# Kernel tuning notes

Measured on AMD Instinct MI355X. Metric: run time of the kernel, lower is better.

## Reference

```python
import math
import jax, jax.numpy as jnp
import numpy as np
from jax.scipy.special import xlogy, gammaln

HEADS = 8
DIM_KEY = 64
NUM_REL_POS_FEATURES = 192


def get_positional_embed(n, feature_size):
    # distances: [-n+1, ..., n-1], length 2n-1
    dist = jnp.arange(-n + 1, n)
    adist = jnp.abs(dist).astype(jnp.float32)[:, None]  # (2n-1, 1)
    num_basis = feature_size // 6  # 3 feature fns * 2 (sign-augmented)
    seq_len = n
    # exponential half-life features
    max_range = math.log(seq_len) / math.log(2.0)
    half_life = 2.0 ** jnp.linspace(3.0, max_range, num_basis)  # min_half_life=3.0
    feat_exp = jnp.exp(-math.log(2.0) / half_life[None, :] * adist)
    # central mask features
    center_widths = 2.0 ** jnp.arange(1, num_basis + 1) - 1.0
    feat_cm = (center_widths[None, :] > adist).astype(jnp.float32)
    # gamma pdf features
    stddev = seq_len / (2 * num_basis)
    start_mean = seq_len / num_basis
    mean = jnp.linspace(start_mean, float(seq_len), num_basis)[None, :]
    concentration = (mean / stddev) ** 2
    rate = mean / (stddev ** 2)
    log_unnorm = xlogy(concentration - 1.0, adist) - rate * adist
    log_norm = gammaln(concentration) - concentration * jnp.log(rate)
    prob = jnp.exp(log_unnorm - log_norm) + 1e-8
    feat_gamma = prob / jnp.max(prob, axis=-1, keepdims=True)
    emb = jnp.concatenate([feat_exp, feat_cm, feat_gamma], axis=-1)  # (2n-1, fs/2)
    sign = jnp.sign(dist).astype(jnp.float32)[:, None]
    return jnp.concatenate([emb, sign * emb], axis=-1)  # (2n-1, fs)


def relative_shift(x):
    # x: (b, h, n, 2n-1) -> (b, h, n, n) Transformer-XL shift
    b, h, t1, t2 = x.shape
    x = jnp.pad(x, ((0, 0), (0, 0), (0, 0), (1, 0)))  # (b,h,t1,t2+1)
    x = x.reshape(b, h, t2 + 1, t1)[:, :, 1:, :].reshape(b, h, t1, t2)
    return x[..., : (t2 + 2) // 2]


def setup_inputs() -> dict:
    key = jax.random.key(0)
    ks = jax.random.split(key, 8)
    dim = 1536
    b, n = 2, 1536
    hdk = HEADS * DIM_KEY  # 512
    hdv = HEADS * 192      # 1536
    s = 0.02
    return {
        'x': jax.random.normal(ks[0], (b, n, dim), jnp.float32),
        'Wq': jax.random.normal(ks[1], (hdk, dim), jnp.float32) * s,
        'Wk': jax.random.normal(ks[2], (hdk, dim), jnp.float32) * s,
        'Wv': jax.random.normal(ks[3], (hdv, dim), jnp.float32) * s,
        'Wrel': jax.random.normal(ks[4], (hdk, NUM_REL_POS_FEATURES), jnp.float32) * s,
        'Wout': jax.random.normal(ks[5], (dim, hdv), jnp.float32) * s,
        'b_out': jnp.zeros((dim,), jnp.float32),
        'rel_content_bias': jax.random.normal(ks[6], (1, HEADS, 1, DIM_KEY), jnp.float32),
        'rel_pos_bias': jax.random.normal(ks[7], (1, HEADS, 1, DIM_KEY), jnp.float32),
    }


def reference(x, Wq, Wk, Wv, Wrel, Wout, b_out, rel_content_bias, rel_pos_bias):
    b, n, dim = x.shape
    h = HEADS
    scale = DIM_KEY ** -0.5

    def split_heads(t):  # (b, n, h*d) -> (b, h, n, d)
        return t.reshape(b, n, h, -1).transpose(0, 2, 1, 3)

    q = split_heads(jnp.einsum('bnd,fd->bnf', x, Wq)) * scale
    k = split_heads(jnp.einsum('bnd,fd->bnf', x, Wk))
    v = split_heads(jnp.einsum('bnd,fd->bnf', x, Wv))

    content_logits = jnp.einsum('bhid,bhjd->bhij', q + rel_content_bias, k)

    positions = get_positional_embed(n, NUM_REL_POS_FEATURES)  # (2n-1, fs)
    rel_k = jnp.einsum('jf,ef->je', positions, Wrel).reshape(2 * n - 1, h, DIM_KEY)
    rel_k = rel_k.transpose(1, 0, 2)  # (h, 2n-1, dk)
    rel_logits = jnp.einsum('bhid,hjd->bhij', q + rel_pos_bias, rel_k)
    rel_logits = relative_shift(rel_logits)  # (b, h, n, n)

    attn = jax.nn.softmax(content_logits + rel_logits, axis=-1)
    out = jnp.einsum('bhij,bhjd->bhid', attn, v)
    out = out.transpose(0, 2, 1, 3).reshape(b, n, -1)  # (b, n, h*dv)
    return jnp.einsum('bnf,df->bnd', out, Wout) + b_out
```

## Files before the change

### kernel.cpp

```cpp
#include <hip/hip_runtime.h>
#include <cmath>

typedef unsigned short u16;
typedef unsigned int u32;
typedef short frag8 __attribute__((ext_vector_type(8)));
typedef float f32x4 __attribute__((ext_vector_type(4)));

#define DEVINL __device__ __forceinline__

DEVINL float bf2f(u16 v) { return __uint_as_float(((u32)v) << 16); }
DEVINL u16 f2bf(float f) {
    u32 u = __float_as_uint(f);
    u32 r = (u + 0x7fffu + ((u >> 16) & 1u)) >> 16;
    return (u16)r;
}
DEVINL u32 pack2(float a, float b) { return (u32)f2bf(a) | ((u32)f2bf(b) << 16); }
DEVINL void async_copy16(const u16* g, u16* l) {
    __builtin_amdgcn_global_load_lds((const __attribute__((address_space(1))) u32*)g,
                                     (__attribute__((address_space(3))) u32*)l, 16, 0, 0);
}
DEVINL f32x4 mfma_bf16(frag8 a, frag8 b, f32x4 c) {
    return __builtin_amdgcn_mfma_f32_16x16x32_bf16(a, b, c, 0, 0, 0);
}

__global__ __launch_bounds__(256) void convert_kernel(
        const float* __restrict__ s0, const float* __restrict__ s1,
        const float* __restrict__ s2, const float* __restrict__ s3,
        const float* __restrict__ s4, u16* __restrict__ dst) {
    const int c0 = 589824, c1 = 98304, c2 = 98304, c3 = 294912;
    const int total = 1376256;
    for (int c = blockIdx.x * blockDim.x + threadIdx.x; c < total;
         c += gridDim.x * blockDim.x) {
        const float* src; int off;
        if (c < c0) { src = s0; off = c; }
        else if (c < c0 + c1) { src = s1; off = c - c0; }
        else if (c < c0 + c1 + c2) { src = s2; off = c - c0 - c1; }
        else if (c < c0 + c1 + c2 + c3) { src = s3; off = c - c0 - c1 - c2; }
        else { src = s4; off = c - c0 - c1 - c2 - c3; }
        float4 a = ((const float4*)src)[off * 2];
        float4 b = ((const float4*)src)[off * 2 + 1];
        uint4 o;
        o.x = pack2(a.x, a.y); o.y = pack2(a.z, a.w);
        o.z = pack2(b.x, b.y); o.w = pack2(b.z, b.w);
        ((uint4*)dst)[c] = o;
    }
}

DEVINL double lgamma_stirling(double z) {
    double zi = 1.0 / z, zi2 = zi * zi;
    return (z - 0.5) * log(z) - z + 0.91893853320467274178
         + zi * (1.0 / 12.0) - zi * zi2 * (1.0 / 360.0) + zi * zi2 * zi2 * (1.0 / 1260.0);
}

__global__ __launch_bounds__(256) void embed_relk_kernel(const float* __restrict__ Wrel,
                                                         u16* __restrict__ relk) {
    __shared__ float pos[16][192];
    __shared__ float inv_hl[32], cwid[32], cm1[32], rateS[32];
    __shared__ double lognS[32];
    __shared__ float gmax[16];
    int t = threadIdx.x;
    int u0b = blockIdx.x * 16;

    if (t < 32) {
        double step = (10.584962500721156 - 3.0) / 31.0;
        double hl = exp2(3.0 + t * step);
        inv_hl[t] = (float)(1.0 / hl);
        cwid[t] = exp2f((float)(t + 1)) - 1.0f;
        double mean = 48.0 * (t + 1);
        double conc = (mean / 24.0) * (mean / 24.0);
        double rate = mean / 576.0;
        cm1[t] = (float)(conc - 1.0);
        rateS[t] = (float)rate;
        lognS[t] = lgamma_stirling(conc) - conc * log(rate);
    }
    __syncthreads();

    for (int idx = t; idx < 512; idx += 256) {
        int ul = idx >> 5, bs = idx & 31;
        int dist = u0b + ul - 1535;
        float ad = fabsf((float)dist);
        pos[ul][bs] = exp2f(-ad * inv_hl[bs]);
        pos[ul][32 + bs] = (cwid[bs] > ad) ? 1.0f : 0.0f;
        double prob = 0.0;
        if (dist != 0) {
            double adD = (double)ad;
            prob = exp((double)cm1[bs] * log(adD) - (double)rateS[bs] * adD - lognS[bs]);
        }
        pos[ul][64 + bs] = (float)(prob + 1e-8);
    }
    __syncthreads();
    if (t < 16) {
        float g = 0.f;
        #pragma unroll
        for (int bsx = 0; bsx < 32; bsx++) g = fmaxf(g, pos[t][64 + bsx]);
        gmax[t] = g;
    }
    __syncthreads();
    for (int idx = t; idx < 16 * 96; idx += 256) {
        int ul = idx / 96, f = idx - ul * 96;
        float v = pos[ul][f];
        if (f >= 64) { v = v / gmax[ul]; pos[ul][f] = v; }
        int dist = u0b + ul - 1535;
        float sg = (dist > 0) ? 1.f : ((dist < 0) ? -1.f : 0.f);
        pos[ul][96 + f] = sg * v;
    }
    __syncthreads();

    int e0 = t * 2;
    const float* w0 = Wrel + e0 * 192;
    const float* w1 = w0 + 192;
    float a0[16], a1[16];
    #pragma unroll
    for (int ul = 0; ul < 16; ul++) { a0[ul] = 0.f; a1[ul] = 0.f; }
    for (int f = 0; f < 192; f++) {
        float wa = w0[f], wb = w1[f];
        #pragma unroll
        for (int ul = 0; ul < 16; ul++) {
            float p = pos[ul][f];
            a0[ul] = fmaf(p, wa, a0[ul]);
            a1[ul] = fmaf(p, wb, a1[ul]);
        }
    }
    int h0 = e0 >> 6, d0 = e0 & 63;
    int h1 = (e0 + 1) >> 6, d1 = (e0 + 1) & 63;
    for (int ul = 0; ul < 16; ul++) {
        int u = u0b + ul;
        relk[(h0 * 3072 + u) * 64 + d0] = f2bf(a0[ul]);
        relk[(h1 * 3072 + u) * 64 + d1] = f2bf(a1[ul]);
    }
}

DEVINL void gemm128_mainloop(const u16* __restrict__ A, const u16* __restrict__ B,
                             int K, f32x4 acc[4][4], u16* As, u16* Bs) {
    int tid = threadIdx.x;
    int lane = tid & 63, wave = tid >> 6;
    int wm = (wave >> 1) * 64, wn = (wave & 1) * 64;
    int fm = lane & 15, fq = lane >> 4;
    for (int k0 = 0; k0 < K; k0 += 32) {
        #pragma unroll
        for (int p = 0; p < 2; p++) {
            int e = (p * 256 + tid) * 8;
            int r = e >> 5, c = e & 31;
            async_copy16(A + r * K + k0 + c, As + e);
            async_copy16(B + r * K + k0 + c, Bs + e);
        }
        __syncthreads();
        frag8 af[4], bfr[4];
        #pragma unroll
        for (int mi = 0; mi < 4; mi++) af[mi] = *(const frag8*)&As[(wm + 16 * mi + fm) * 32 + fq * 8];
        #pragma unroll
        for (int ni = 0; ni < 4; ni++) bfr[ni] = *(const frag8*)&Bs[(wn + 16 * ni + fm) * 32 + fq * 8];
        #pragma unroll
        for (int mi = 0; mi < 4; mi++)
            #pragma unroll
            for (int ni = 0; ni < 4; ni++)
                acc[mi][ni] = mfma_bf16(af[mi], bfr[ni], acc[mi][ni]);
        __syncthreads();
    }
}

__global__ __launch_bounds__(256) void gemm_qkv_kernel(
        const u16* __restrict__ X, const u16* __restrict__ Wq, const u16* __restrict__ Wk,
        const u16* __restrict__ Wv, const float* __restrict__ cbias, const float* __restrict__ pbias,
        u16* __restrict__ qc, u16* __restrict__ qp, u16* __restrict__ kws, u16* __restrict__ vt) {
    __shared__ __align__(16) u16 As[128 * 32];
    __shared__ __align__(16) u16 Bs[128 * 32];
    int m0 = blockIdx.x * 128, n0 = blockIdx.y * 128;
    const u16* Bp; int brow;
    if (n0 < 512)       { Bp = Wq; brow = n0; }
    else if (n0 < 1024) { Bp = Wk; brow = n0 - 512; }
    else                { Bp = Wv; brow = n0 - 1024; }
    f32x4 acc[4][4];
    #pragma unroll
    for (int i = 0; i < 4; i++)
        #pragma unroll
        for (int j = 0; j < 4; j++) acc[i][j] = (f32x4){0.f, 0.f, 0.f, 0.f};
    gemm128_mainloop(X + m0 * 1536, Bp + brow * 1536, 1536, acc, As, Bs);

    int tid = threadIdx.x, lane = tid & 63, wave = tid >> 6;
    int wm = (wave >> 1) * 64, wn = (wave & 1) * 64, fm = lane & 15, fq = lane >> 4;
    #pragma unroll
    for (int mi = 0; mi < 4; mi++) {
        #pragma unroll
        for (int ni = 0; ni < 4; ni++) {
            int col = n0 + wn + 16 * ni + fm;
            int rbase = m0 + wm + 16 * mi + fq * 4;
            #pragma unroll
            for (int reg = 0; reg < 4; reg++) {
                int row = rbase + reg;
                float v = acc[mi][ni][reg];
                int b = row >= 1536 ? 1 : 0;
                int i = row - b * 1536;
                if (n0 < 512) {
                    float qv = v * 0.125f;
                    int idx = ((b * 8 + (col >> 6)) * 1536 + i) * 64 + (col & 63);
                    qc[idx] = f2bf(qv + cbias[col]);
                    qp[idx] = f2bf(qv + pbias[col]);
                } else if (n0 < 1024) {
                    int c2 = col - 512;
                    kws[((b * 8 + (c2 >> 6)) * 1536 + i) * 64 + (c2 & 63)] = f2bf(v);
                } else {
                    int c2 = col - 1024;
                    int hh = c2 / 192, dd = c2 - hh * 192;
                    vt[((b * 8 + hh) * 192 + dd) * 1536 + i] = f2bf(v);
                }
            }
        }
    }
}

__global__ __launch_bounds__(256) void attn_kernel(
        const u16* __restrict__ qc, const u16* __restrict__ qp, const u16* __restrict__ kws,
        const u16* __restrict__ vt, const u16* __restrict__ relk, u16* __restrict__ ao) {
    __shared__ __align__(16) u16 smem[24768];
    u16* k_lds    = smem;
    u16* vt_lds   = smem + 4096;
    u16* relk_lds = smem + 16384;
    u16* P_lds    = smem + 22528;
    float* S_lds  = (float*)k_lds;
    float* R_lds  = (float*)relk_lds;
    float* mstate = (float*)(smem + 24576);
    float* lstate = mstate + 32;
    float* alpha_lds = lstate + 32;

    const int n = 1536;
    int bh = blockIdx.y, b = bh >> 3, h = bh & 7;
    int i0 = blockIdx.x * 32;
    const u16* qcP = qc + bh * n * 64;
    const u16* qpP = qp + bh * n * 64;
    const u16* kP  = kws + bh * n * 64;
    const u16* vtP = vt + bh * 192 * n;
    const u16* rkP = relk + h * 3072 * 64;

    int tid = threadIdx.x, lane = tid & 63, w = tid >> 6, fm = lane & 15, fq = lane >> 4;
    int sw = fm & 7;
    if (tid < 32) { mstate[tid] = __int_as_float(0xff800000); lstate[tid] = 0.f; }

    frag8 aqc[2][2], aqp[2][2];
    #pragma unroll
    for (int mi = 0; mi < 2; mi++)
        #pragma unroll
        for (int ks = 0; ks < 2; ks++) {
            int off = (i0 + 16 * mi + fm) * 64 + ks * 32 + fq * 8;
            aqc[mi][ks] = *(const frag8*)(qcP + off);
            aqp[mi][ks] = *(const frag8*)(qpP + off);
        }

    f32x4 acc_o[2][3];
    #pragma unroll
    for (int mi = 0; mi < 2; mi++)
        #pragma unroll
        for (int dj = 0; dj < 3; dj++) acc_o[mi][dj] = (f32x4){0.f, 0.f, 0.f, 0.f};

    int uis[3], rmis[3];
    #pragma unroll
    for (int tt = 0; tt < 3; tt++) {
        int tv = w + tt * 4;
        rmis[tt] = (tv >= 6) ? 1 : 0;
        uis[tt] = tv - rmis[tt] * 6;
    }

    for (int jt = 0; jt < 24; jt++) {
        int j0 = jt * 64;
        __syncthreads();
        #pragma unroll
        for (int p = 0; p < 2; p++) {
            int l = p * 256 + tid, r = l >> 3, c = (l & 7) ^ (r & 7);
            async_copy16(kP + (j0 + r) * 64 + c * 8, k_lds + l * 8);
        }
        #pragma unroll
        for (int p = 0; p < 6; p++) {
            int l = p * 256 + tid, r = l >> 3, c = (l & 7) ^ (r & 7);
            async_copy16(vtP + r * n + j0 + c * 8, vt_lds + l * 8);
        }
        int u0 = 1504 + j0 - i0;
        #pragma unroll
        for (int p = 0; p < 3; p++) {
            int l = p * 256 + tid, r = l >> 3, c = (l & 7) ^ (r & 7);
            async_copy16(rkP + (u0 + r) * 64 + c * 8, relk_lds + l * 8);
        }
        __syncthreads();

        f32x4 acc_s[2];
        acc_s[0] = (f32x4){0.f, 0.f, 0.f, 0.f};
        acc_s[1] = (f32x4){0.f, 0.f, 0.f, 0.f};
        #pragma unroll
        for (int ks = 0; ks < 2; ks++) {
            frag8 bk = *(const frag8*)&k_lds[(16 * w + fm) * 64 + ((ks * 4 + fq) ^ sw) * 8];
            acc_s[0] = mfma_bf16(aqc[0][ks], bk, acc_s[0]);
            acc_s[1] = mfma_bf16(aqc[1][ks], bk, acc_s[1]);
        }
        f32x4 acc_r[3];
        #pragma unroll
        for (int tt = 0; tt < 3; tt++) {
            acc_r[tt] = (f32x4){0.f, 0.f, 0.f, 0.f};
            #pragma unroll
            for (int ks = 0; ks < 2; ks++) {
                frag8 br = *(const frag8*)&relk_lds[(16 * uis[tt] + fm) * 64 + ((ks * 4 + fq) ^ sw) * 8];
                acc_r[tt] = mfma_bf16(aqp[rmis[tt]][ks], br, acc_r[tt]);
            }
        }
        __syncthreads();

        #pragma unroll
        for (int mi = 0; mi < 2; mi++)
            #pragma unroll
            for (int reg = 0; reg < 4; reg++)
                S_lds[(16 * mi + fq * 4 + reg) * 64 + 16 * w + fm] = acc_s[mi][reg];
        #pragma unroll
        for (int tt = 0; tt < 3; tt++)
            #pragma unroll
            for (int reg = 0; reg < 4; reg++)
                R_lds[(16 * rmis[tt] + fq * 4 + reg) * 96 + 16 * uis[tt] + fm] = acc_r[tt][reg];
        __syncthreads();

        int li = tid >> 3, c0 = (tid & 7) * 8;
        float sv[8];
        float mx = __int_as_float(0xff800000);
        #pragma unroll
        for (int e = 0; e < 8; e++) {
            int c = c0 + e;
            sv[e] = S_lds[li * 64 + c] + R_lds[li * 96 + c - li + 31];
            mx = fmaxf(mx, sv[e]);
        }
        mx = fmaxf(mx, __shfl_xor(mx, 1));
        mx = fmaxf(mx, __shfl_xor(mx, 2));
        mx = fmaxf(mx, __shfl_xor(mx, 4));
        float mo = mstate[li];
        float mn = fmaxf(mo, mx);
        float al = __expf(mo - mn);
        float pe[8], sum = 0.f;
        #pragma unroll
        for (int e = 0; e < 8; e++) { pe[e] = __expf(sv[e] - mn); sum += pe[e]; }
        {
            uint4 pw;
            pw.x = pack2(pe[0], pe[1]); pw.y = pack2(pe[2], pe[3]);
            pw.z = pack2(pe[4], pe[5]); pw.w = pack2(pe[6], pe[7]);
            int slot = (tid & 7) ^ (li & 7);
            *(uint4*)&P_lds[li * 64 + slot * 8] = pw;
        }
        sum += __shfl_xor(sum, 1);
        sum += __shfl_xor(sum, 2);
        sum += __shfl_xor(sum, 4);
        if ((tid & 7) == 0) {
            mstate[li] = mn;
            lstate[li] = lstate[li] * al + sum;
            alpha_lds[li] = al;
        }
        __syncthreads();

        #pragma unroll
        for (int mi = 0; mi < 2; mi++)
            #pragma unroll
            for (int reg = 0; reg < 4; reg++) {
                float al2 = alpha_lds[16 * mi + fq * 4 + reg];
                #pragma unroll
                for (int dj = 0; dj < 3; dj++) acc_o[mi][dj][reg] *= al2;
            }
        frag8 ap[2][2];
        #pragma unroll
        for (int mi = 0; mi < 2; mi++)
            #pragma unroll
            for (int ks = 0; ks < 2; ks++)
                ap[mi][ks] = *(const frag8*)&P_lds[(16 * mi + fm) * 64 + ((ks * 4 + fq) ^ sw) * 8];
        #pragma unroll
        for (int dj = 0; dj < 3; dj++) {
            #pragma unroll
            for (int ks = 0; ks < 2; ks++) {
                frag8 bv = *(const frag8*)&vt_lds[(16 * (3 * w + dj) + fm) * 64 + ((ks * 4 + fq) ^ sw) * 8];
                acc_o[0][dj] = mfma_bf16(ap[0][ks], bv, acc_o[0][dj]);
                acc_o[1][dj] = mfma_bf16(ap[1][ks], bv, acc_o[1][dj]);
            }
        }
    }

    __syncthreads();
    #pragma unroll
    for (int mi = 0; mi < 2; mi++)
        #pragma unroll
        for (int dj = 0; dj < 3; dj++)
            #pragma unroll
            for (int reg = 0; reg < 4; reg++) {
                int rl = 16 * mi + fq * 4 + reg;
                float lsum = lstate[rl];
                int row = b * 1536 + i0 + rl;
                int col = h * 192 + 16 * (3 * w + dj) + fm;
                ao[row * 1536 + col] = f2bf(acc_o[mi][dj][reg] / lsum);
            }
}

__global__ __launch_bounds__(256) void gemm_out_kernel(
        const u16* __restrict__ A, const u16* __restrict__ W, const float* __restrict__ bias,
        float* __restrict__ out) {
    __shared__ __align__(16) u16 As[128 * 32];
    __shared__ __align__(16) u16 Bs[128 * 32];
    int m0 = blockIdx.x * 128, n0 = blockIdx.y * 128;
    f32x4 acc[4][4];
    #pragma unroll
    for (int i = 0; i < 4; i++)
        #pragma unroll
        for (int j = 0; j < 4; j++) acc[i][j] = (f32x4){0.f, 0.f, 0.f, 0.f};
    gemm128_mainloop(A + m0 * 1536, W + n0 * 1536, 1536, acc, As, Bs);

    int tid = threadIdx.x, lane = tid & 63, wave = tid >> 6;
    int wm = (wave >> 1) * 64, wn = (wave & 1) * 64, fm = lane & 15, fq = lane >> 4;
    #pragma unroll
    for (int mi = 0; mi < 4; mi++) {
        #pragma unroll
        for (int ni = 0; ni < 4; ni++) {
            int col = n0 + wn + 16 * ni + fm;
            int rbase = m0 + wm + 16 * mi + fq * 4;
            float bv = bias[col];
            #pragma unroll
            for (int reg = 0; reg < 4; reg++) {
                int row = rbase + reg;
                out[row * 1536 + col] = acc[mi][ni][reg] + bv;
            }
        }
    }
}

extern "C" void kernel_launch(void* const* d_in, const int* in_sizes, int n_in,
                              void* d_out, int out_size, void* d_ws, size_t ws_size,
                              hipStream_t stream) {
    (void)in_sizes; (void)n_in; (void)out_size; (void)ws_size;
    const float* x    = (const float*)d_in[0];
    const float* Wq   = (const float*)d_in[1];
    const float* Wk   = (const float*)d_in[2];
    const float* Wv   = (const float*)d_in[3];
    const float* Wrel = (const float*)d_in[4];
    const float* Wout = (const float*)d_in[5];
    const float* bout = (const float*)d_in[6];
    const float* cb   = (const float*)d_in[7];
    const float* pb   = (const float*)d_in[8];

    u16* xb  = (u16*)d_ws;
    u16* wqb = xb  + 4718592;
    u16* wkb = wqb + 786432;
    u16* wvb = wkb + 786432;
    u16* wob = wvb + 2359296;
    u16* qc  = wob + 2359296;
    u16* qp  = qc + 1572864;
    u16* kw  = qp + 1572864;
    u16* vt  = kw + 1572864;
    u16* rk  = vt + 4718592;
    u16* ao  = rk + 1572864;
    float* out = (float*)d_out;

    convert_kernel<<<dim3(1024), dim3(256), 0, stream>>>(x, Wq, Wk, Wv, Wout, xb);
    embed_relk_kernel<<<dim3(192), dim3(256), 0, stream>>>(Wrel, rk);
    gemm_qkv_kernel<<<dim3(24, 20), dim3(256), 0, stream>>>(xb, wqb, wkb, wvb, cb, pb, qc, qp, kw, vt);
    attn_kernel<<<dim3(48, 16), dim3(256), 0, stream>>>(qc, qp, kw, vt, rk, ao);
    gemm_out_kernel<<<dim3(24, 12), dim3(256), 0, stream>>>(ao, wob, bout, out);
}
```

Measured before the change: 328.2 us.

## Read attention operands directly from global, stage V transpose via LDS, shrink output GEMM tile

The attention kernel drops its LDS staging of K, V^T and rel-K tiles and loads MFMA fragments straight from global memory. It also keeps softmax max/sum state in registers, using cross-wave LDS reductions, which removes the S_lds round trip. The QKV GEMM now writes the transposed V output through an LDS tile so stores are 16-byte coalesced instead of scattered 2-byte writes. The output GEMM moves to a 64x128 tile, giving twice as many blocks for better CU occupancy. Direct global fragment loads depend on cache hits and may stall more than the async LDS copies did.

```diff
diff --git a/kernel.cpp b/kernel.cpp
--- a/kernel.cpp
+++ b/kernel.cpp
@@ -163,8 +163,9 @@
         const u16* __restrict__ X, const u16* __restrict__ Wq, const u16* __restrict__ Wk,
         const u16* __restrict__ Wv, const float* __restrict__ cbias, const float* __restrict__ pbias,
         u16* __restrict__ qc, u16* __restrict__ qp, u16* __restrict__ kws, u16* __restrict__ vt) {
-    __shared__ __align__(16) u16 As[128 * 32];
-    __shared__ __align__(16) u16 Bs[128 * 32];
+    __shared__ __align__(16) u16 smem[8192];
+    u16* As = smem;
+    u16* Bs = smem + 4096;
     int m0 = blockIdx.x * 128, n0 = blockIdx.y * 128;
     const u16* Bp; int brow;
     if (n0 < 512)       { Bp = Wq; brow = n0; }
@@ -179,32 +180,54 @@
 
     int tid = threadIdx.x, lane = tid & 63, wave = tid >> 6;
     int wm = (wave >> 1) * 64, wn = (wave & 1) * 64, fm = lane & 15, fq = lane >> 4;
-    #pragma unroll
-    for (int mi = 0; mi < 4; mi++) {
-        #pragma unroll
-        for (int ni = 0; ni < 4; ni++) {
-            int col = n0 + wn + 16 * ni + fm;
-            int rbase = m0 + wm + 16 * mi + fq * 4;
-            #pragma unroll
-            for (int reg = 0; reg < 4; reg++) {
-                int row = rbase + reg;
-                float v = acc[mi][ni][reg];
-                int b = row >= 1536 ? 1 : 0;
-                int i = row - b * 1536;
-                if (n0 < 512) {
-                    float qv = v * 0.125f;
-                    int idx = ((b * 8 + (col >> 6)) * 1536 + i) * 64 + (col & 63);
-                    qc[idx] = f2bf(qv + cbias[col]);
-                    qp[idx] = f2bf(qv + pbias[col]);
-                } else if (n0 < 1024) {
-                    int c2 = col - 512;
-                    kws[((b * 8 + (c2 >> 6)) * 1536 + i) * 64 + (c2 & 63)] = f2bf(v);
-                } else {
-                    int c2 = col - 1024;
-                    int hh = c2 / 192, dd = c2 - hh * 192;
-                    vt[((b * 8 + hh) * 192 + dd) * 1536 + i] = f2bf(v);
+
+    if (n0 < 1024) {
+        #pragma unroll
+        for (int mi = 0; mi < 4; mi++) {
+            #pragma unroll
+            for (int ni = 0; ni < 4; ni++) {
+                int col = n0 + wn + 16 * ni + fm;
+                int rbase = m0 + wm + 16 * mi + fq * 4;
+                #pragma unroll
+                for (int reg = 0; reg < 4; reg++) {
+                    int row = rbase + reg;
+                    float v = acc[mi][ni][reg];
+                    int b = row >= 1536 ? 1 : 0;
+                    int i = row - b * 1536;
+                    if (n0 < 512) {
+                        float qv = v * 0.125f;
+                        int idx = ((b * 8 + (col >> 6)) * 1536 + i) * 64 + (col & 63);
+                        qc[idx] = f2bf(qv + cbias[col]);
+                        qp[idx] = f2bf(qv + pbias[col]);
+                    } else {
+                        int c2 = col - 512;
+                        kws[((b * 8 + (c2 >> 6)) * 1536 + i) * 64 + (c2 & 63)] = f2bf(v);
+                    }
                 }
             }
+        }
+    } else {
+        u16* T = smem;
+        #pragma unroll
+        for (int mi = 0; mi < 4; mi++) {
+            if (mi) __syncthreads();
+            #pragma unroll
+            for (int ni = 0; ni < 4; ni++)
+                #pragma unroll
+                for (int reg = 0; reg < 4; reg++)
+                    T[(wn + 16 * ni + fm) * 34 + (wave >> 1) * 16 + fq * 4 + reg] =
+                        f2bf(acc[mi][ni][reg]);
+            __syncthreads();
+            int c = tid >> 1, half = tid & 1;
+            int col = n0 - 1024 + c;
+            int hh = col / 192, dd = col - hh * 192;
+            int ibase = m0 + half * 64 + 16 * mi;
+            int b = ibase >= 1536 ? 1 : 0;
+            int il = ibase - b * 1536;
+            u16* dstp = vt + ((b * 8 + hh) * 192 + dd) * 1536 + il;
+            const u16* srcp = &T[c * 34 + half * 16];
+            *(uint4*)dstp = *(const uint4*)srcp;
+            *(uint4*)(dstp + 8) = *(const uint4*)(srcp + 8);
         }
     }
 }
@@ -212,16 +235,9 @@
 __global__ __launch_bounds__(256) void attn_kernel(
         const u16* __restrict__ qc, const u16* __restrict__ qp, const u16* __restrict__ kws,
         const u16* __restrict__ vt, const u16* __restrict__ relk, u16* __restrict__ ao) {
-    __shared__ __align__(16) u16 smem[24768];
-    u16* k_lds    = smem;
-    u16* vt_lds   = smem + 4096;
-    u16* relk_lds = smem + 16384;
-    u16* P_lds    = smem + 22528;
-    float* S_lds  = (float*)k_lds;
-    float* R_lds  = (float*)relk_lds;
-    float* mstate = (float*)(smem + 24576);
-    float* lstate = mstate + 32;
-    float* alpha_lds = lstate + 32;
+    __shared__ float R_lds[32 * 96];
+    __shared__ __align__(16) u16 P_lds[32 * 64];
+    __shared__ float pmax[4 * 32], psum[4 * 32];
 
     const int n = 1536;
     int bh = blockIdx.y, b = bh >> 3, h = bh & 7;
@@ -232,9 +248,9 @@
     const u16* vtP = vt + bh * 192 * n;
     const u16* rkP = relk + h * 3072 * 64;
 
-    int tid = threadIdx.x, lane = tid & 63, w = tid >> 6, fm = lane & 15, fq = lane >> 4;
+    int tid = threadIdx.x, fm = tid & 15, fq = (tid >> 4) & 3, w = tid >> 6;
+    int jl = 16 * w + fm;
     int sw = fm & 7;
-    if (tid < 32) { mstate[tid] = __int_as_float(0xff800000); lstate[tid] = 0.f; }
 
     frag8 aqc[2][2], aqp[2][2];
     #pragma unroll
@@ -251,6 +267,9 @@
     for (int mi = 0; mi < 2; mi++)
         #pragma unroll
         for (int dj = 0; dj < 3; dj++) acc_o[mi][dj] = (f32x4){0.f, 0.f, 0.f, 0.f};
+    float mst[8], lst[8];
+    #pragma unroll
+    for (int k = 0; k < 8; k++) { mst[k] = __int_as_float(0xff800000); lst[k] = 0.f; }
 
     int uis[3], rmis[3];
     #pragma unroll
@@ -262,101 +281,88 @@
 
     for (int jt = 0; jt < 24; jt++) {
         int j0 = jt * 64;
-        __syncthreads();
-        #pragma unroll
-        for (int p = 0; p < 2; p++) {
-            int l = p * 256 + tid, r = l >> 3, c = (l & 7) ^ (r & 7);
-            async_copy16(kP + (j0 + r) * 64 + c * 8, k_lds + l * 8);
-        }
-        #pragma unroll
-        for (int p = 0; p < 6; p++) {
-            int l = p * 256 + tid, r = l >> 3, c = (l & 7) ^ (r & 7);
-            async_copy16(vtP + r * n + j0 + c * 8, vt_lds + l * 8);
-        }
         int u0 = 1504 + j0 - i0;
-        #pragma unroll
-        for (int p = 0; p < 3; p++) {
-            int l = p * 256 + tid, r = l >> 3, c = (l & 7) ^ (r & 7);
-            async_copy16(rkP + (u0 + r) * 64 + c * 8, relk_lds + l * 8);
-        }
-        __syncthreads();
 
         f32x4 acc_s[2];
         acc_s[0] = (f32x4){0.f, 0.f, 0.f, 0.f};
         acc_s[1] = (f32x4){0.f, 0.f, 0.f, 0.f};
         #pragma unroll
         for (int ks = 0; ks < 2; ks++) {
-            frag8 bk = *(const frag8*)&k_lds[(16 * w + fm) * 64 + ((ks * 4 + fq) ^ sw) * 8];
+            frag8 bk = *(const frag8*)&kP[(j0 + jl) * 64 + ks * 32 + fq * 8];
             acc_s[0] = mfma_bf16(aqc[0][ks], bk, acc_s[0]);
             acc_s[1] = mfma_bf16(aqc[1][ks], bk, acc_s[1]);
         }
-        f32x4 acc_r[3];
         #pragma unroll
         for (int tt = 0; tt < 3; tt++) {
-            acc_r[tt] = (f32x4){0.f, 0.f, 0.f, 0.f};
+            f32x4 r = (f32x4){0.f, 0.f, 0.f, 0.f};
             #pragma unroll
             for (int ks = 0; ks < 2; ks++) {
-                frag8 br = *(const frag8*)&relk_lds[(16 * uis[tt] + fm) * 64 + ((ks * 4 + fq) ^ sw) * 8];
-                acc_r[tt] = mfma_bf16(aqp[rmis[tt]][ks], br, acc_r[tt]);
-            }
-        }
-        __syncthreads();
-
+                frag8 br = *(const frag8*)&rkP[(u0 + 16 * uis[tt] + fm) * 64 + ks * 32 + fq * 8];
+                r = mfma_bf16(aqp[rmis[tt]][ks], br, r);
+            }
+            #pragma unroll
+            for (int reg = 0; reg < 4; reg++)
+                R_lds[(16 * rmis[tt] + fq * 4 + reg) * 96 + 16 * uis[tt] + fm] = r[reg];
+        }
+        __syncthreads();
+
+        float sv[8], pm[8];
         #pragma unroll
         for (int mi = 0; mi < 2; mi++)
             #pragma unroll
-            for (int reg = 0; reg < 4; reg++)
-                S_lds[(16 * mi + fq * 4 + reg) * 64 + 16 * w + fm] = acc_s[mi][reg];
-        #pragma unroll
-        for (int tt = 0; tt < 3; tt++)
-            #pragma unroll
-            for (int reg = 0; reg < 4; reg++)
-                R_lds[(16 * rmis[tt] + fq * 4 + reg) * 96 + 16 * uis[tt] + fm] = acc_r[tt][reg];
-        __syncthreads();
-
-        int li = tid >> 3, c0 = (tid & 7) * 8;
-        float sv[8];
-        float mx = __int_as_float(0xff800000);
-        #pragma unroll
-        for (int e = 0; e < 8; e++) {
-            int c = c0 + e;
-            sv[e] = S_lds[li * 64 + c] + R_lds[li * 96 + c - li + 31];
-            mx = fmaxf(mx, sv[e]);
-        }
-        mx = fmaxf(mx, __shfl_xor(mx, 1));
-        mx = fmaxf(mx, __shfl_xor(mx, 2));
-        mx = fmaxf(mx, __shfl_xor(mx, 4));
-        float mo = mstate[li];
-        float mn = fmaxf(mo, mx);
-        float al = __expf(mo - mn);
-        float pe[8], sum = 0.f;
-        #pragma unroll
-        for (int e = 0; e < 8; e++) { pe[e] = __expf(sv[e] - mn); sum += pe[e]; }
-        {
-            uint4 pw;
-            pw.x = pack2(pe[0], pe[1]); pw.y = pack2(pe[2], pe[3]);
-            pw.z = pack2(pe[4], pe[5]); pw.w = pack2(pe[6], pe[7]);
-            int slot = (tid & 7) ^ (li & 7);
-            *(uint4*)&P_lds[li * 64 + slot * 8] = pw;
-        }
-        sum += __shfl_xor(sum, 1);
-        sum += __shfl_xor(sum, 2);
-        sum += __shfl_xor(sum, 4);
-        if ((tid & 7) == 0) {
-            mstate[li] = mn;
-            lstate[li] = lstate[li] * al + sum;
-            alpha_lds[li] = al;
-        }
-        __syncthreads();
-
+            for (int reg = 0; reg < 4; reg++) {
+                int il = 16 * mi + 4 * fq + reg;
+                float v = acc_s[mi][reg] + R_lds[il * 96 + jl - il + 31];
+                sv[mi * 4 + reg] = v;
+                pm[mi * 4 + reg] = v;
+            }
+        #pragma unroll
+        for (int d = 1; d < 16; d <<= 1)
+            #pragma unroll
+            for (int k = 0; k < 8; k++) pm[k] = fmaxf(pm[k], __shfl_xor(pm[k], d));
+        if (fm == 0) {
+            #pragma unroll
+            for (int k = 0; k < 8; k++)
+                pmax[w * 32 + 16 * (k >> 2) + 4 * fq + (k & 3)] = pm[k];
+        }
+        __syncthreads();
+
+        float alv[8], ps[8];
+        #pragma unroll
+        for (int k = 0; k < 8; k++) {
+            int i = 16 * (k >> 2) + 4 * fq + (k & 3);
+            float mx = fmaxf(fmaxf(pmax[i], pmax[32 + i]), fmaxf(pmax[64 + i], pmax[96 + i]));
+            float mn = fmaxf(mst[k], mx);
+            alv[k] = __expf(mst[k] - mn);
+            mst[k] = mn;
+            float pe = __expf(sv[k] - mn);
+            ps[k] = pe;
+            P_lds[i * 64 + (((jl >> 3) ^ (i & 7)) << 3) + (jl & 7)] = f2bf(pe);
+        }
+        #pragma unroll
+        for (int d = 1; d < 16; d <<= 1)
+            #pragma unroll
+            for (int k = 0; k < 8; k++) ps[k] += __shfl_xor(ps[k], d);
+        if (fm == 0) {
+            #pragma unroll
+            for (int k = 0; k < 8; k++)
+                psum[w * 32 + 16 * (k >> 2) + 4 * fq + (k & 3)] = ps[k];
+        }
         #pragma unroll
         for (int mi = 0; mi < 2; mi++)
             #pragma unroll
             for (int reg = 0; reg < 4; reg++) {
-                float al2 = alpha_lds[16 * mi + fq * 4 + reg];
+                float a = alv[mi * 4 + reg];
                 #pragma unroll
-                for (int dj = 0; dj < 3; dj++) acc_o[mi][dj][reg] *= al2;
-            }
+                for (int dj = 0; dj < 3; dj++) acc_o[mi][dj][reg] *= a;
+            }
+        __syncthreads();
+
+        #pragma unroll
+        for (int k = 0; k < 8; k++) {
+            int i = 16 * (k >> 2) + 4 * fq + (k & 3);
+            lst[k] = lst[k] * alv[k] + (psum[i] + psum[32 + i] + psum[64 + i] + psum[96 + i]);
+        }
         frag8 ap[2][2];
         #pragma unroll
         for (int mi = 0; mi < 2; mi++)
@@ -367,45 +373,72 @@
         for (int dj = 0; dj < 3; dj++) {
             #pragma unroll
             for (int ks = 0; ks < 2; ks++) {
-                frag8 bv = *(const frag8*)&vt_lds[(16 * (3 * w + dj) + fm) * 64 + ((ks * 4 + fq) ^ sw) * 8];
+                frag8 bv = *(const frag8*)&vtP[(16 * (3 * w + dj) + fm) * n + j0 + ks * 32 + fq * 8];
                 acc_o[0][dj] = mfma_bf16(ap[0][ks], bv, acc_o[0][dj]);
                 acc_o[1][dj] = mfma_bf16(ap[1][ks], bv, acc_o[1][dj]);
             }
         }
     }
 
-    __syncthreads();
     #pragma unroll
     for (int mi = 0; mi < 2; mi++)
         #pragma unroll
-        for (int dj = 0; dj < 3; dj++)
-            #pragma unroll
-            for (int reg = 0; reg < 4; reg++) {
-                int rl = 16 * mi + fq * 4 + reg;
-                float lsum = lstate[rl];
-                int row = b * 1536 + i0 + rl;
+        for (int reg = 0; reg < 4; reg++) {
+            int i = 16 * mi + 4 * fq + reg;
+            float inv = 1.0f / lst[mi * 4 + reg];
+            int row = b * 1536 + i0 + i;
+            #pragma unroll
+            for (int dj = 0; dj < 3; dj++) {
                 int col = h * 192 + 16 * (3 * w + dj) + fm;
-                ao[row * 1536 + col] = f2bf(acc_o[mi][dj][reg] / lsum);
-            }
+                ao[row * 1536 + col] = f2bf(acc_o[mi][dj][reg] * inv);
+            }
+        }
 }
 
 __global__ __launch_bounds__(256) void gemm_out_kernel(
         const u16* __restrict__ A, const u16* __restrict__ W, const float* __restrict__ bias,
         float* __restrict__ out) {
-    __shared__ __align__(16) u16 As[128 * 32];
+    __shared__ __align__(16) u16 As[64 * 32];
     __shared__ __align__(16) u16 Bs[128 * 32];
-    int m0 = blockIdx.x * 128, n0 = blockIdx.y * 128;
-    f32x4 acc[4][4];
-    #pragma unroll
-    for (int i = 0; i < 4; i++)
+    int m0 = blockIdx.x * 64, n0 = blockIdx.y * 128;
+    int tid = threadIdx.x, lane = tid & 63, wave = tid >> 6;
+    int wm = (wave & 1) * 32, wn = (wave >> 1) * 64;
+    int fm = lane & 15, fq = lane >> 4;
+    const u16* Ab = A + m0 * 1536;
+    const u16* Wb = W + n0 * 1536;
+    f32x4 acc[2][4];
+    #pragma unroll
+    for (int i = 0; i < 2; i++)
         #pragma unroll
         for (int j = 0; j < 4; j++) acc[i][j] = (f32x4){0.f, 0.f, 0.f, 0.f};
-    gemm128_mainloop(A + m0 * 1536, W + n0 * 1536, 1536, acc, As, Bs);
-
-    int tid = threadIdx.x, lane = tid & 63, wave = tid >> 6;
-    int wm = (wave >> 1) * 64, wn = (wave & 1) * 64, fm = lane & 15, fq = lane >> 4;
-    #pragma unroll
-    for (int mi = 0; mi < 4; mi++) {
+
+    for (int k0 = 0; k0 < 1536; k0 += 32) {
+        {
+            int r = tid >> 2, c = (tid & 3) * 8;
+            async_copy16(Ab + r * 1536 + k0 + c, As + tid * 8);
+        }
+        #pragma unroll
+        for (int p = 0; p < 2; p++) {
+            int e = (p * 256 + tid) * 8;
+            int r = e >> 5, c = e & 31;
+            async_copy16(Wb + r * 1536 + k0 + c, Bs + e);
+        }
+        __syncthreads();
+        frag8 af[2], bfr[4];
+        #pragma unroll
+        for (int mi = 0; mi < 2; mi++) af[mi] = *(const frag8*)&As[(wm + 16 * mi + fm) * 32 + fq * 8];
+        #pragma unroll
+        for (int ni = 0; ni < 4; ni++) bfr[ni] = *(const frag8*)&Bs[(wn + 16 * ni + fm) * 32 + fq * 8];
+        #pragma unroll
+        for (int mi = 0; mi < 2; mi++)
+            #pragma unroll
+            for (int ni = 0; ni < 4; ni++)
+                acc[mi][ni] = mfma_bf16(af[mi], bfr[ni], acc[mi][ni]);
+        __syncthreads();
+    }
+
+    #pragma unroll
+    for (int mi = 0; mi < 2; mi++) {
         #pragma unroll
         for (int ni = 0; ni < 4; ni++) {
             int col = n0 + wn + 16 * ni + fm;
@@ -451,5 +484,5 @@
     embed_relk_kernel<<<dim3(192), dim3(256), 0, stream>>>(Wrel, rk);
     gemm_qkv_kernel<<<dim3(24, 20), dim3(256), 0, stream>>>(xb, wqb, wkb, wvb, cb, pb, qc, qp, kw, vt);
     attn_kernel<<<dim3(48, 16), dim3(256), 0, stream>>>(qc, qp, kw, vt, rk, ao);
-    gemm_out_kernel<<<dim3(24, 12), dim3(256), 0, stream>>>(ao, wob, bout, out);
-}
+    gemm_out_kernel<<<dim3(48, 12), dim3(256), 0, stream>>>(ao, wob, bout, out);
+}
```

Result: slower. 393.7 us (+19.9%).
